# Kernel tuning notes

Measured on AMD Instinct MI355X. Metric: run time of the kernel, lower is better.

Reference implementation:

```python
import jax, jax.numpy as jnp
import numpy as np

D = 1024      # input_dim == output_dim
H = 2048      # hidden_dimension per expert
E = 8         # num_experts
K = 2         # top-k
B, T = 4, 2048


def setup_inputs() -> dict:
    key = jax.random.key(0)
    ks = jax.random.split(key, 7)
    s = 0.02
    return {
        "x":  jax.random.normal(ks[0], (B, T, D), dtype=jnp.float32),
        "W1": jax.random.normal(ks[1], (E, D, 2 * H), dtype=jnp.float32) * s,
        "b1": jnp.zeros((E, 2 * H), dtype=jnp.float32),
        "W2": jax.random.normal(ks[2], (E, H, D), dtype=jnp.float32) * s,
        "b2": jnp.zeros((E, D), dtype=jnp.float32),
        "Wr": jax.random.normal(ks[3], (D, E), dtype=jnp.float32) * s,
        "br": jnp.zeros((E,), dtype=jnp.float32),
    }


def reference(x, W1, b1, W2, b2, Wr, br):
    Bb, Tt, Dd = x.shape
    xf = x.reshape(-1, Dd)                      # [N, D]

    # Router: top-k logits, softmax over the k selected logits
    logits = xf @ Wr + br                       # [N, E]
    topk_val, topk_idx = jax.lax.top_k(logits, K)   # [N, K]
    scores = jax.nn.softmax(topk_val, axis=-1)      # [N, K]

    # Dense expert compute (same math as original: every expert sees all tokens)
    h = jnp.einsum('nd,edh->enh', xf, W1) + b1[:, None, :]   # [E, N, 2H]
    a, g = jnp.split(h, 2, axis=-1)                          # swiglu halves
    act = jax.nn.silu(a) * g                                 # [E, N, H]
    out_e = jnp.einsum('enh,ehd->end', act, W2) + b2[:, None, :]  # [E, N, D]

    # Combine: gather each token's top-k expert outputs and weight by scores
    out_ne = out_e.transpose(1, 0, 2)                        # [N, E, D]
    gathered = jnp.take_along_axis(out_ne, topk_idx[:, :, None], axis=1)  # [N, K, D]
    out = jnp.sum(gathered * scores[:, :, None], axis=1)     # [N, D]
    return out.reshape(Bb, Tt, Dd)
```

## Files before the change

kernel.cpp:

```cpp
#include <hip/hip_runtime.h>
#include <stdint.h>

#define N_TOK   8192
#define DIM     1024
#define HID     2048
#define TWOH    4096
#define NEXP    8
#define CAP     8192
#define CAP_A   3072
#define NSLOT   (N_TOK * 2)

typedef __bf16 bf16x8 __attribute__((ext_vector_type(8)));
typedef float  f32x4  __attribute__((ext_vector_type(4)));

__device__ __forceinline__ uint16_t f2bf(float f) {
  union { float f; uint32_t u; } v; v.f = f;
  uint32_t u = v.u;
  return (uint16_t)((u + 0x7fffu + ((u >> 16) & 1u)) >> 16);
}

__device__ __forceinline__ float bf2f(uint16_t h) {
  union { uint32_t u; float f; } v; v.u = ((uint32_t)h) << 16;
  return v.f;
}

__device__ __forceinline__ void gl2lds16(const void* g, void* l) {
  __builtin_amdgcn_global_load_lds(
      (const __attribute__((address_space(1))) void*)g,
      (__attribute__((address_space(3))) void*)l, 16, 0, 0);
}

__global__ __launch_bounds__(256)
void transpose_cvt_kernel(const float* __restrict__ in, uint16_t* __restrict__ out,
                          int R, int C) {
  __shared__ float tile[64][33];
  size_t zoff = (size_t)blockIdx.z * (size_t)R * C;
  int c0 = blockIdx.x * 32, r0 = blockIdx.y * 64;
  int tid = threadIdx.x;
  int lr = tid >> 3;
  int lc = (tid & 7) * 4;
#pragma unroll
  for (int rr = 0; rr < 2; ++rr) {
    int r = lr + rr * 32;
    float4 v = *(const float4*)&in[zoff + (size_t)(r0 + r) * C + c0 + lc];
    tile[r][lc + 0] = v.x; tile[r][lc + 1] = v.y;
    tile[r][lc + 2] = v.z; tile[r][lc + 3] = v.w;
  }
  __syncthreads();
  int cc = tid >> 3;
  int rb = (tid & 7) * 8;
  union { ushort4 u4[2]; uint16_t s[8]; } pk;
#pragma unroll
  for (int j = 0; j < 8; ++j) pk.s[j] = f2bf(tile[rb + j][cc]);
  ushort4* dst = (ushort4*)&out[zoff + (size_t)(c0 + cc) * R + r0 + rb];
  dst[0] = pk.u4[0];
  dst[1] = pk.u4[1];
}

__global__ __launch_bounds__(256)
void wr_transpose_kernel(const float* __restrict__ Wr, float* __restrict__ WrT) {
  int i = blockIdx.x * 256 + threadIdx.x;
  int d = i >> 3, e = i & 7;
  WrT[e * DIM + d] = Wr[i];
}

__global__ __launch_bounds__(256)
void router_kernel(const float* __restrict__ x, const float* __restrict__ WrT,
                   const float* __restrict__ br, float* __restrict__ scores,
                   int* __restrict__ eids, uint16_t* __restrict__ xb) {
  int tok  = blockIdx.x * 4 + (threadIdx.x >> 6);
  int lane = threadIdx.x & 63;
  size_t xbase = (size_t)tok * DIM;

  float xv[16];
#pragma unroll
  for (int j = 0; j < 4; ++j) {
    int d0 = j * 256 + lane * 4;
    float4 v = *(const float4*)&x[xbase + d0];
    ushort4 pk;
    pk.x = f2bf(v.x); pk.y = f2bf(v.y); pk.z = f2bf(v.z); pk.w = f2bf(v.w);
    *(ushort4*)&xb[xbase + d0] = pk;
    xv[j * 4 + 0] = v.x; xv[j * 4 + 1] = v.y;
    xv[j * 4 + 2] = v.z; xv[j * 4 + 3] = v.w;
  }

  double acc[NEXP];
#pragma unroll
  for (int e = 0; e < NEXP; ++e) acc[e] = 0.0;
#pragma unroll
  for (int e = 0; e < NEXP; ++e) {
#pragma unroll
    for (int j = 0; j < 4; ++j) {
      int d0 = j * 256 + lane * 4;
      float4 w = *(const float4*)&WrT[e * DIM + d0];
      acc[e] += (double)xv[j * 4 + 0] * (double)w.x;
      acc[e] += (double)xv[j * 4 + 1] * (double)w.y;
      acc[e] += (double)xv[j * 4 + 2] * (double)w.z;
      acc[e] += (double)xv[j * 4 + 3] * (double)w.w;
    }
  }
#pragma unroll
  for (int e = 0; e < NEXP; ++e) {
#pragma unroll
    for (int m = 32; m > 0; m >>= 1) acc[e] += __shfl_xor(acc[e], m, 64);
  }
  if (lane == 0) {
    double lg[NEXP];
#pragma unroll
    for (int e = 0; e < NEXP; ++e) lg[e] = acc[e] + (double)br[e];
    int i0 = 0;
#pragma unroll
    for (int e = 1; e < NEXP; ++e) if (lg[e] > lg[i0]) i0 = e;
    int i1 = (i0 == 0) ? 1 : 0;
#pragma unroll
    for (int e = 0; e < NEXP; ++e) if (e != i0 && lg[e] > lg[i1]) i1 = e;
    double ex = exp(lg[i1] - lg[i0]);
    scores[tok * 2 + 0] = (float)(1.0 / (1.0 + ex));
    scores[tok * 2 + 1] = (float)(ex / (1.0 + ex));
    eids[tok * 2 + 0] = i0;
    eids[tok * 2 + 1] = i1;
  }
}

__global__ __launch_bounds__(256)
void build_lists_kernel(const int* __restrict__ eids, int* __restrict__ lists,
                        int* __restrict__ counts) {
  int e = blockIdx.x;
  int tid = threadIdx.x, lane = tid & 63, w = tid >> 6;
  __shared__ int wcnt[4];
  int base = 0;
  for (int c = 0; c < NSLOT; c += 256) {
    int s = c + tid;
    int match = (eids[s] == e) ? 1 : 0;
    unsigned long long m = __ballot(match);
    int wtot = __popcll(m);
    int rank = __popcll(m & ((1ull << lane) - 1ull));
    if (lane == 0) wcnt[w] = wtot;
    __syncthreads();
    int pre = 0;
#pragma unroll
    for (int i = 0; i < 4; ++i) pre += (i < w) ? wcnt[i] : 0;
    int tot = wcnt[0] + wcnt[1] + wcnt[2] + wcnt[3];
    if (match) lists[e * CAP + base + pre + rank] = s;
    base += tot;
    __syncthreads();
  }
  if (tid == 0) counts[e] = base;
}

__global__ __launch_bounds__(256, 4)
void gemm1_kernel(const uint16_t* __restrict__ xb,
                  const uint16_t* __restrict__ W1t,
                  const float* __restrict__ b1,
                  const int* __restrict__ lists, const int* __restrict__ counts,
                  uint16_t* __restrict__ act)
{
  int e = blockIdx.z;
  int cnt = counts[e];
  int mtile = blockIdx.y;
  if (mtile * 128 >= cnt) return;
  int jt = blockIdx.x;

  __shared__ __align__(16) uint16_t As[2 * 4096];
  __shared__ __align__(16) uint16_t Bs[2 * 4096];
  __shared__ int ent[128];

  int tid = threadIdx.x, lane = tid & 63, w = tid >> 6;
  if (tid < 128) {
    int gi = mtile * 128 + tid;
    ent[tid] = lists[e * CAP + (gi < cnt ? gi : 0)];
  }
  __syncthreads();

  const uint16_t* agp[2];
  const uint16_t* bgp[2];
  uint16_t* alds[2];
  uint16_t* blds[2];
#pragma unroll
  for (int r = 0; r < 2; ++r) {
    int row  = (w * 2 + r) * 16 + (lane >> 2);
    int c    = (((lane & 3) - (row >> 2)) & 3) * 8;
    int slot = ent[row];
    agp[r] = xb + (size_t)(slot >> 1) * DIM + c;
    int grow = (row < 64) ? (jt * 64 + row) : (HID + jt * 64 + (row - 64));
    bgp[r] = W1t + ((size_t)e * TWOH + grow) * DIM + c;
    alds[r] = &As[(w * 2 + r) * 512];
    blds[r] = &Bs[(w * 2 + r) * 512];
  }

  f32x4 zero = {0.f, 0.f, 0.f, 0.f};
  f32x4 acc_a[4][2], acc_g[4][2];
#pragma unroll
  for (int i = 0; i < 4; ++i)
#pragma unroll
    for (int j = 0; j < 2; ++j) { acc_a[i][j] = zero; acc_g[i][j] = zero; }

  int qd = lane >> 4, l15 = lane & 15;
  int wm = w >> 1, wn = w & 1;
  int sl = ((qd + (l15 >> 2)) & 3) * 8;

#pragma unroll
  for (int r = 0; r < 2; ++r) { gl2lds16(agp[r], alds[r]); gl2lds16(bgp[r], blds[r]); }

  for (int it = 0; it < DIM / 32; ++it) {
    __syncthreads();
    int nk = (it + 1) * 32;
    int nb = ((it + 1) & 1) * 4096;
    if (nk < DIM) {
#pragma unroll
      for (int r = 0; r < 2; ++r) {
        gl2lds16(agp[r] + nk, alds[r] + nb);
        gl2lds16(bgp[r] + nk, blds[r] + nb);
      }
    }
    int cb = (it & 1) * 4096;
    bf16x8 af[4], ba[2], bg[2];
#pragma unroll
    for (int i = 0; i < 4; ++i)
      af[i] = *(const bf16x8*)&As[cb + (wm * 64 + i * 16 + l15) * 32 + sl];
#pragma unroll
    for (int j = 0; j < 2; ++j) {
      int brow = wn * 32 + j * 16 + l15;
      ba[j] = *(const bf16x8*)&Bs[cb + brow * 32 + sl];
      bg[j] = *(const bf16x8*)&Bs[cb + (brow + 64) * 32 + sl];
    }
#pragma unroll
    for (int i = 0; i < 4; ++i)
#pragma unroll
      for (int j = 0; j < 2; ++j) {
        acc_a[i][j] = __builtin_amdgcn_mfma_f32_16x16x32_bf16(af[i], ba[j], acc_a[i][j], 0, 0, 0);
        acc_g[i][j] = __builtin_amdgcn_mfma_f32_16x16x32_bf16(af[i], bg[j], acc_g[i][j], 0, 0, 0);
      }
  }

#pragma unroll
  for (int i = 0; i < 4; ++i) {
#pragma unroll
    for (int rr = 0; rr < 4; ++rr) {
      int row = wm * 64 + i * 16 + qd * 4 + rr;
      int gidx = mtile * 128 + row;
      if (gidx >= cnt || gidx >= CAP_A) continue;
#pragma unroll
      for (int j = 0; j < 2; ++j) {
        int col = jt * 64 + wn * 32 + j * 16 + l15;
        float a = acc_a[i][j][rr] + b1[e * TWOH + col];
        float g = acc_g[i][j][rr] + b1[e * TWOH + HID + col];
        float s = a / (1.f + __expf(-a));
        act[((size_t)e * CAP_A + gidx) * HID + col] = f2bf(s * g);
      }
    }
  }
}

__global__ __launch_bounds__(256, 4)
void gemm2_kernel(const uint16_t* __restrict__ act,
                  const uint16_t* __restrict__ W2t,
                  const float* __restrict__ b2,
                  const float* __restrict__ scores,
                  const int* __restrict__ lists, const int* __restrict__ counts,
                  uint16_t* __restrict__ tmp)
{
  int e = blockIdx.z;
  int cnt = counts[e];
  int mtile = blockIdx.y;
  if (mtile * 128 >= cnt) return;
  int nbase = blockIdx.x * 128;

  __shared__ __align__(16) uint16_t As[2 * 4096];
  __shared__ __align__(16) uint16_t Bs[2 * 4096];
  __shared__ int ent[128];

  int tid = threadIdx.x, lane = tid & 63, w = tid >> 6;
  if (tid < 128) {
    int gi = mtile * 128 + tid;
    ent[tid] = lists[e * CAP + (gi < cnt ? gi : 0)];
  }

  const uint16_t* agp[2];
  const uint16_t* bgp[2];
  uint16_t* alds[2];
  uint16_t* blds[2];
#pragma unroll
  for (int r = 0; r < 2; ++r) {
    int row  = (w * 2 + r) * 16 + (lane >> 2);
    int c    = (((lane & 3) - (row >> 2)) & 3) * 8;
    agp[r] = act + ((size_t)e * CAP_A + mtile * 128 + row) * HID + c;
    bgp[r] = W2t + ((size_t)e * DIM + nbase + row) * HID + c;
    alds[r] = &As[(w * 2 + r) * 512];
    blds[r] = &Bs[(w * 2 + r) * 512];
  }

  f32x4 zero = {0.f, 0.f, 0.f, 0.f};
  f32x4 acc[4][4];
#pragma unroll
  for (int i = 0; i < 4; ++i)
#pragma unroll
    for (int j = 0; j < 4; ++j) acc[i][j] = zero;

  int qd = lane >> 4, l15 = lane & 15;
  int wm = w >> 1, wn = w & 1;
  int sl = ((qd + (l15 >> 2)) & 3) * 8;

#pragma unroll
  for (int r = 0; r < 2; ++r) { gl2lds16(agp[r], alds[r]); gl2lds16(bgp[r], blds[r]); }

  for (int it = 0; it < HID / 32; ++it) {
    __syncthreads();
    int nk = (it + 1) * 32;
    int nb = ((it + 1) & 1) * 4096;
    if (nk < HID) {
#pragma unroll
      for (int r = 0; r < 2; ++r) {
        gl2lds16(agp[r] + nk, alds[r] + nb);
        gl2lds16(bgp[r] + nk, blds[r] + nb);
      }
    }
    int cb = (it & 1) * 4096;
    bf16x8 af[4], bf_[4];
#pragma unroll
    for (int i = 0; i < 4; ++i)
      af[i] = *(const bf16x8*)&As[cb + (wm * 64 + i * 16 + l15) * 32 + sl];
#pragma unroll
    for (int j = 0; j < 4; ++j)
      bf_[j] = *(const bf16x8*)&Bs[cb + (wn * 64 + j * 16 + l15) * 32 + sl];
#pragma unroll
    for (int i = 0; i < 4; ++i)
#pragma unroll
      for (int j = 0; j < 4; ++j)
        acc[i][j] = __builtin_amdgcn_mfma_f32_16x16x32_bf16(af[i], bf_[j], acc[i][j], 0, 0, 0);
  }

#pragma unroll
  for (int i = 0; i < 4; ++i) {
#pragma unroll
    for (int rr = 0; rr < 4; ++rr) {
      int row = wm * 64 + i * 16 + qd * 4 + rr;
      if (mtile * 128 + row >= cnt) continue;
      int slot = ent[row];
      float sw = scores[slot];
#pragma unroll
      for (int j = 0; j < 4; ++j) {
        int col = nbase + wn * 64 + j * 16 + l15;
        float v = (acc[i][j][rr] + b2[e * DIM + col]) * sw;
        tmp[(size_t)slot * DIM + col] = f2bf(v);
      }
    }
  }
}

__global__ void combine_kernel(const uint16_t* __restrict__ tmp, float* __restrict__ out) {
  int i = blockIdx.x * blockDim.x + threadIdx.x;
  int n = i >> 8;
  int d = (i & 255) * 4;
  const ushort4 a = *(const ushort4*)&tmp[(size_t)(2 * n) * DIM + d];
  const ushort4 b = *(const ushort4*)&tmp[(size_t)(2 * n + 1) * DIM + d];
  float4 o;
  o.x = bf2f(a.x) + bf2f(b.x);
  o.y = bf2f(a.y) + bf2f(b.y);
  o.z = bf2f(a.z) + bf2f(b.z);
  o.w = bf2f(a.w) + bf2f(b.w);
  *(float4*)&out[(size_t)n * DIM + d] = o;
}

extern "C" void kernel_launch(void* const* d_in, const int* in_sizes, int n_in,
                              void* d_out, int out_size, void* d_ws, size_t ws_size,
                              hipStream_t stream) {
  const float* x  = (const float*)d_in[0];
  const float* W1 = (const float*)d_in[1];
  const float* b1 = (const float*)d_in[2];
  const float* W2 = (const float*)d_in[3];
  const float* b2 = (const float*)d_in[4];
  const float* Wr = (const float*)d_in[5];
  const float* br = (const float*)d_in[6];
  float* out = (float*)d_out;
  (void)in_sizes; (void)n_in; (void)ws_size; (void)out_size;

  char* ws = (char*)d_ws;
  size_t off = 0;
  auto alloc = [&](size_t bytes) {
    char* p = ws + off;
    off += (bytes + 255) & ~(size_t)255;
    return p;
  };
  uint16_t* xb     = (uint16_t*)alloc((size_t)N_TOK * DIM * 2);
  uint16_t* W1t    = (uint16_t*)alloc((size_t)NEXP * TWOH * DIM * 2);
  uint16_t* W2t    = (uint16_t*)alloc((size_t)NEXP * DIM * HID * 2);
  uint16_t* actb   = (uint16_t*)alloc((size_t)NEXP * CAP_A * HID * 2);
  float*    scores = (float*)alloc((size_t)NSLOT * 4);
  int*      lists  = (int*)alloc((size_t)NEXP * CAP * 4);
  int*      counts = (int*)alloc(256);
  float*    WrT    = (float*)alloc((size_t)NEXP * DIM * 4);
  int*      eids   = (int*)alloc((size_t)NSLOT * 4);
  uint16_t* tmpb   = W1t;

  wr_transpose_kernel<<<(NEXP * DIM) / 256, 256, 0, stream>>>(Wr, WrT);
  router_kernel<<<N_TOK / 4, 256, 0, stream>>>(x, WrT, br, scores, eids, xb);
  build_lists_kernel<<<NEXP, 256, 0, stream>>>(eids, lists, counts);
  transpose_cvt_kernel<<<dim3(TWOH / 32, DIM / 64, NEXP), 256, 0, stream>>>(W1, W1t, DIM, TWOH);
  transpose_cvt_kernel<<<dim3(DIM / 32, HID / 64, NEXP), 256, 0, stream>>>(W2, W2t, HID, DIM);
  gemm1_kernel<<<dim3(HID / 64, CAP_A / 128, NEXP), 256, 0, stream>>>(xb, W1t, b1, lists, counts, actb);
  gemm2_kernel<<<dim3(DIM / 128, CAP_A / 128, NEXP), 256, 0, stream>>>(actb, W2t, b2, scores, lists, counts, tmpb);
  combine_kernel<<<(N_TOK * DIM / 4) / 256, 256, 0, stream>>>(tmpb, out);
}
```

Baseline: 658.7 us.

## Triple-buffer LDS tiles in both expert GEMMs with two-stage prefetch

Both grouped GEMM kernels now keep three LDS buffers per operand and prefetch two K-slices ahead. Each iteration uses a partial vmcnt wait plus a raw barrier instead of a full __syncthreads, so global-to-LDS loads overlap more MFMA work. The cost is 50% more LDS per block and a lower occupancy target (3 blocks per CU instead of 4). The final iterations issue wrap-around dummy loads into an unused buffer, and gemm2 gains an explicit sync after the entry list is filled.

```diff
diff --git a/kernel.cpp b/kernel.cpp
--- a/kernel.cpp
+++ b/kernel.cpp
@@ -148,7 +148,7 @@
   if (tid == 0) counts[e] = base;
 }
 
-__global__ __launch_bounds__(256, 4)
+__global__ __launch_bounds__(256, 3)
 void gemm1_kernel(const uint16_t* __restrict__ xb,
                   const uint16_t* __restrict__ W1t,
                   const float* __restrict__ b1,
@@ -161,8 +161,8 @@
   if (mtile * 128 >= cnt) return;
   int jt = blockIdx.x;
 
-  __shared__ __align__(16) uint16_t As[2 * 4096];
-  __shared__ __align__(16) uint16_t Bs[2 * 4096];
+  __shared__ __align__(16) uint16_t As[3 * 4096];
+  __shared__ __align__(16) uint16_t Bs[3 * 4096];
   __shared__ int ent[128];
 
   int tid = threadIdx.x, lane = tid & 63, w = tid >> 6;
@@ -200,29 +200,33 @@
   int sl = ((qd + (l15 >> 2)) & 3) * 8;
 
 #pragma unroll
-  for (int r = 0; r < 2; ++r) { gl2lds16(agp[r], alds[r]); gl2lds16(bgp[r], blds[r]); }
-
+  for (int r = 0; r < 2; ++r) {
+    gl2lds16(agp[r], alds[r]);            gl2lds16(bgp[r], blds[r]);
+    gl2lds16(agp[r] + 32, alds[r] + 4096); gl2lds16(bgp[r] + 32, blds[r] + 4096);
+  }
+
+  int co = 0, so = 2 * 4096;
   for (int it = 0; it < DIM / 32; ++it) {
-    __syncthreads();
-    int nk = (it + 1) * 32;
-    int nb = ((it + 1) & 1) * 4096;
-    if (nk < DIM) {
-#pragma unroll
-      for (int r = 0; r < 2; ++r) {
-        gl2lds16(agp[r] + nk, alds[r] + nb);
-        gl2lds16(bgp[r] + nk, blds[r] + nb);
-      }
-    }
-    int cb = (it & 1) * 4096;
+    asm volatile("s_waitcnt vmcnt(4)" ::: "memory");
+    __builtin_amdgcn_s_barrier();
+    __builtin_amdgcn_sched_barrier(0);
+    int st = it + 2;
+    if (st >= DIM / 32) st -= DIM / 32;
+    int nk = st * 32;
+#pragma unroll
+    for (int r = 0; r < 2; ++r) {
+      gl2lds16(agp[r] + nk, alds[r] + so);
+      gl2lds16(bgp[r] + nk, blds[r] + so);
+    }
     bf16x8 af[4], ba[2], bg[2];
 #pragma unroll
     for (int i = 0; i < 4; ++i)
-      af[i] = *(const bf16x8*)&As[cb + (wm * 64 + i * 16 + l15) * 32 + sl];
+      af[i] = *(const bf16x8*)&As[co + (wm * 64 + i * 16 + l15) * 32 + sl];
 #pragma unroll
     for (int j = 0; j < 2; ++j) {
       int brow = wn * 32 + j * 16 + l15;
-      ba[j] = *(const bf16x8*)&Bs[cb + brow * 32 + sl];
-      bg[j] = *(const bf16x8*)&Bs[cb + (brow + 64) * 32 + sl];
+      ba[j] = *(const bf16x8*)&Bs[co + brow * 32 + sl];
+      bg[j] = *(const bf16x8*)&Bs[co + (brow + 64) * 32 + sl];
     }
 #pragma unroll
     for (int i = 0; i < 4; ++i)
@@ -231,6 +235,8 @@
         acc_a[i][j] = __builtin_amdgcn_mfma_f32_16x16x32_bf16(af[i], ba[j], acc_a[i][j], 0, 0, 0);
         acc_g[i][j] = __builtin_amdgcn_mfma_f32_16x16x32_bf16(af[i], bg[j], acc_g[i][j], 0, 0, 0);
       }
+    co = (co == 2 * 4096) ? 0 : co + 4096;
+    so = (so == 2 * 4096) ? 0 : so + 4096;
   }
 
 #pragma unroll
@@ -252,7 +258,7 @@
   }
 }
 
-__global__ __launch_bounds__(256, 4)
+__global__ __launch_bounds__(256, 3)
 void gemm2_kernel(const uint16_t* __restrict__ act,
                   const uint16_t* __restrict__ W2t,
                   const float* __restrict__ b2,
@@ -266,8 +272,8 @@
   if (mtile * 128 >= cnt) return;
   int nbase = blockIdx.x * 128;
 
-  __shared__ __align__(16) uint16_t As[2 * 4096];
-  __shared__ __align__(16) uint16_t Bs[2 * 4096];
+  __shared__ __align__(16) uint16_t As[3 * 4096];
+  __shared__ __align__(16) uint16_t Bs[3 * 4096];
   __shared__ int ent[128];
 
   int tid = threadIdx.x, lane = tid & 63, w = tid >> 6;
@@ -275,6 +281,7 @@
     int gi = mtile * 128 + tid;
     ent[tid] = lists[e * CAP + (gi < cnt ? gi : 0)];
   }
+  __syncthreads();
 
   const uint16_t* agp[2];
   const uint16_t* bgp[2];
@@ -302,32 +309,38 @@
   int sl = ((qd + (l15 >> 2)) & 3) * 8;
 
 #pragma unroll
-  for (int r = 0; r < 2; ++r) { gl2lds16(agp[r], alds[r]); gl2lds16(bgp[r], blds[r]); }
-
+  for (int r = 0; r < 2; ++r) {
+    gl2lds16(agp[r], alds[r]);            gl2lds16(bgp[r], blds[r]);
+    gl2lds16(agp[r] + 32, alds[r] + 4096); gl2lds16(bgp[r] + 32, blds[r] + 4096);
+  }
+
+  int co = 0, so = 2 * 4096;
   for (int it = 0; it < HID / 32; ++it) {
-    __syncthreads();
-    int nk = (it + 1) * 32;
-    int nb = ((it + 1) & 1) * 4096;
-    if (nk < HID) {
-#pragma unroll
-      for (int r = 0; r < 2; ++r) {
-        gl2lds16(agp[r] + nk, alds[r] + nb);
-        gl2lds16(bgp[r] + nk, blds[r] + nb);
-      }
-    }
-    int cb = (it & 1) * 4096;
+    asm volatile("s_waitcnt vmcnt(4)" ::: "memory");
+    __builtin_amdgcn_s_barrier();
+    __builtin_amdgcn_sched_barrier(0);
+    int st = it + 2;
+    if (st >= HID / 32) st -= HID / 32;
+    int nk = st * 32;
+#pragma unroll
+    for (int r = 0; r < 2; ++r) {
+      gl2lds16(agp[r] + nk, alds[r] + so);
+      gl2lds16(bgp[r] + nk, blds[r] + so);
+    }
     bf16x8 af[4], bf_[4];
 #pragma unroll
     for (int i = 0; i < 4; ++i)
-      af[i] = *(const bf16x8*)&As[cb + (wm * 64 + i * 16 + l15) * 32 + sl];
+      af[i] = *(const bf16x8*)&As[co + (wm * 64 + i * 16 + l15) * 32 + sl];
 #pragma unroll
     for (int j = 0; j < 4; ++j)
-      bf_[j] = *(const bf16x8*)&Bs[cb + (wn * 64 + j * 16 + l15) * 32 + sl];
+      bf_[j] = *(const bf16x8*)&Bs[co + (wn * 64 + j * 16 + l15) * 32 + sl];
 #pragma unroll
     for (int i = 0; i < 4; ++i)
 #pragma unroll
       for (int j = 0; j < 4; ++j)
         acc[i][j] = __builtin_amdgcn_mfma_f32_16x16x32_bf16(af[i], bf_[j], acc[i][j], 0, 0, 0);
+    co = (co == 2 * 4096) ? 0 : co + 4096;
+    so = (so == 2 * 4096) ? 0 : so + 4096;
   }
 
 #pragma unroll
```

Result: no change. 665.2 us (+1.0%).

## Widen gemm1 tile to 128 hidden columns with 512-thread blocks

Applied to the files above, without the earlier changes.

gemm1 now launches 512-thread blocks, each computing a 128-token by 128-hidden-column tile (with the matching gate columns) instead of 64 columns. The gathered token rows loaded into LDS are reused across twice as many weight columns, and the grid has half as many blocks along the hidden dimension. This raises LDS use per block and increases register pressure per CU. A missing __syncthreads after filling the ent array in gemm2 is also added, which fixes a race.

```diff
diff --git a/kernel.cpp b/kernel.cpp
--- a/kernel.cpp
+++ b/kernel.cpp
@@ -148,7 +148,7 @@
   if (tid == 0) counts[e] = base;
 }
 
-__global__ __launch_bounds__(256, 4)
+__global__ __launch_bounds__(512, 4)
 void gemm1_kernel(const uint16_t* __restrict__ xb,
                   const uint16_t* __restrict__ W1t,
                   const float* __restrict__ b1,
@@ -162,7 +162,7 @@
   int jt = blockIdx.x;
 
   __shared__ __align__(16) uint16_t As[2 * 4096];
-  __shared__ __align__(16) uint16_t Bs[2 * 4096];
+  __shared__ __align__(16) uint16_t Bs[2 * 8192];
   __shared__ int ent[128];
 
   int tid = threadIdx.x, lane = tid & 63, w = tid >> 6;
@@ -172,20 +172,18 @@
   }
   __syncthreads();
 
-  const uint16_t* agp[2];
+  int srow = w * 16 + (lane >> 2);
+  int c    = (((lane & 3) - (srow >> 2)) & 3) * 8;
+  const uint16_t* agp = xb + (size_t)(ent[srow] >> 1) * DIM + c;
+  uint16_t* alds = &As[w * 512];
   const uint16_t* bgp[2];
-  uint16_t* alds[2];
   uint16_t* blds[2];
 #pragma unroll
   for (int r = 0; r < 2; ++r) {
-    int row  = (w * 2 + r) * 16 + (lane >> 2);
-    int c    = (((lane & 3) - (row >> 2)) & 3) * 8;
-    int slot = ent[row];
-    agp[r] = xb + (size_t)(slot >> 1) * DIM + c;
-    int grow = (row < 64) ? (jt * 64 + row) : (HID + jt * 64 + (row - 64));
+    int rb = r * 128 + srow;
+    int grow = (rb < 128) ? (jt * 128 + rb) : (HID + jt * 128 + (rb - 128));
     bgp[r] = W1t + ((size_t)e * TWOH + grow) * DIM + c;
-    alds[r] = &As[(w * 2 + r) * 512];
-    blds[r] = &Bs[(w * 2 + r) * 512];
+    blds[r] = &Bs[r * 4096 + w * 512];
   }
 
   f32x4 zero = {0.f, 0.f, 0.f, 0.f};
@@ -196,33 +194,34 @@
     for (int j = 0; j < 2; ++j) { acc_a[i][j] = zero; acc_g[i][j] = zero; }
 
   int qd = lane >> 4, l15 = lane & 15;
-  int wm = w >> 1, wn = w & 1;
+  int wm = w >> 2, wn = w & 3;
   int sl = ((qd + (l15 >> 2)) & 3) * 8;
 
-#pragma unroll
-  for (int r = 0; r < 2; ++r) { gl2lds16(agp[r], alds[r]); gl2lds16(bgp[r], blds[r]); }
+  gl2lds16(agp, alds);
+  gl2lds16(bgp[0], blds[0]);
+  gl2lds16(bgp[1], blds[1]);
 
   for (int it = 0; it < DIM / 32; ++it) {
     __syncthreads();
     int nk = (it + 1) * 32;
-    int nb = ((it + 1) & 1) * 4096;
     if (nk < DIM) {
-#pragma unroll
-      for (int r = 0; r < 2; ++r) {
-        gl2lds16(agp[r] + nk, alds[r] + nb);
-        gl2lds16(bgp[r] + nk, blds[r] + nb);
-      }
-    }
-    int cb = (it & 1) * 4096;
+      int na  = ((it + 1) & 1) * 4096;
+      int nbb = ((it + 1) & 1) * 8192;
+      gl2lds16(agp + nk, alds + na);
+      gl2lds16(bgp[0] + nk, blds[0] + nbb);
+      gl2lds16(bgp[1] + nk, blds[1] + nbb);
+    }
+    int ca_ = (it & 1) * 4096;
+    int cb_ = (it & 1) * 8192;
     bf16x8 af[4], ba[2], bg[2];
 #pragma unroll
     for (int i = 0; i < 4; ++i)
-      af[i] = *(const bf16x8*)&As[cb + (wm * 64 + i * 16 + l15) * 32 + sl];
+      af[i] = *(const bf16x8*)&As[ca_ + (wm * 64 + i * 16 + l15) * 32 + sl];
 #pragma unroll
     for (int j = 0; j < 2; ++j) {
       int brow = wn * 32 + j * 16 + l15;
-      ba[j] = *(const bf16x8*)&Bs[cb + brow * 32 + sl];
-      bg[j] = *(const bf16x8*)&Bs[cb + (brow + 64) * 32 + sl];
+      ba[j] = *(const bf16x8*)&Bs[cb_ + brow * 32 + sl];
+      bg[j] = *(const bf16x8*)&Bs[cb_ + (brow + 128) * 32 + sl];
     }
 #pragma unroll
     for (int i = 0; i < 4; ++i)
@@ -242,7 +241,7 @@
       if (gidx >= cnt || gidx >= CAP_A) continue;
 #pragma unroll
       for (int j = 0; j < 2; ++j) {
-        int col = jt * 64 + wn * 32 + j * 16 + l15;
+        int col = jt * 128 + wn * 32 + j * 16 + l15;
         float a = acc_a[i][j][rr] + b1[e * TWOH + col];
         float g = acc_g[i][j][rr] + b1[e * TWOH + HID + col];
         float s = a / (1.f + __expf(-a));
@@ -275,6 +274,7 @@
     int gi = mtile * 128 + tid;
     ent[tid] = lists[e * CAP + (gi < cnt ? gi : 0)];
   }
+  __syncthreads();
 
   const uint16_t* agp[2];
   const uint16_t* bgp[2];
@@ -398,7 +398,7 @@
   build_lists_kernel<<<NEXP, 256, 0, stream>>>(eids, lists, counts);
   transpose_cvt_kernel<<<dim3(TWOH / 32, DIM / 64, NEXP), 256, 0, stream>>>(W1, W1t, DIM, TWOH);
   transpose_cvt_kernel<<<dim3(DIM / 32, HID / 64, NEXP), 256, 0, stream>>>(W2, W2t, HID, DIM);
-  gemm1_kernel<<<dim3(HID / 64, CAP_A / 128, NEXP), 256, 0, stream>>>(xb, W1t, b1, lists, counts, actb);
+  gemm1_kernel<<<dim3(HID / 128, CAP_A / 128, NEXP), 512, 0, stream>>>(xb, W1t, b1, lists, counts, actb);
   gemm2_kernel<<<dim3(DIM / 128, CAP_A / 128, NEXP), 256, 0, stream>>>(actb, W2t, b2, scores, lists, counts, tmpb);
   combine_kernel<<<(N_TOK * DIM / 4) / 256, 256, 0, stream>>>(tmpb, out);
 }
```

Result: no change. 663.1 us (+0.7%).
